# Kernel optimization log

Hardware: AMD Instinct MI355X
Metric: run time of the kernel (lower is better)

Reference implementation:

```python
import jax, jax.numpy as jnp
import numpy as np

B, S, DIM, HEADS, HD, FF = 2, 2048, 1024, 16, 64, 4096
PREV, MAX_SEQ, THETA, POS_BIAS_MAX, EPS = 1024, 4096, 10000.0, 2.0, 1e-6


def _freqs_cos_sin():
    inv = 1.0 / THETA ** (np.arange(0, HD, 2)[: HD // 2].astype(np.float32) / HD)
    f = np.outer(np.arange(MAX_SEQ, dtype=np.float32), inv)
    return jnp.asarray(np.cos(f), jnp.float32), jnp.asarray(np.sin(f), jnp.float32)


def setup_inputs():
    key = jax.random.key(0)
    ks = jax.random.split(key, 16)
    lin = lambda k, o, i: 0.02 * jax.random.normal(k, (o, i), jnp.float32)
    cos, sin = _freqs_cos_sin()
    return {
        "x": jax.random.normal(ks[0], (B, S, DIM), jnp.float32),
        "cache_k": jax.random.normal(ks[1], (B, HEADS, PREV, HD), jnp.float32),
        "cache_v": jax.random.normal(ks[2], (B, HEADS, PREV, HD), jnp.float32),
        "cos": cos, "sin": sin,
        "attn_norm_w": jnp.ones((DIM,), jnp.float32),
        "ffn_norm_w": jnp.ones((DIM,), jnp.float32),
        "wq": lin(ks[3], DIM, DIM), "bq": jnp.zeros((DIM,), jnp.float32),
        "wk": lin(ks[4], DIM, DIM), "bk": jnp.zeros((DIM,), jnp.float32),
        "wv": lin(ks[5], DIM, DIM), "bv": jnp.zeros((DIM,), jnp.float32),
        "wo": lin(ks[6], DIM, DIM), "bo": jnp.zeros((DIM,), jnp.float32),
        "w_gate": lin(ks[7], FF, DIM), "b_gate": jnp.zeros((FF,), jnp.float32),
        "w_value": lin(ks[8], FF, DIM), "b_value": jnp.zeros((FF,), jnp.float32),
        "w_proj": lin(ks[9], DIM, FF), "b_proj": jnp.zeros((DIM,), jnp.float32),
        "cache_limit": 3072,
    }


def _rmsnorm(h, w):
    return h * jax.lax.rsqrt(jnp.mean(h * h, axis=-1, keepdims=True) + EPS) * w


def _rope(t, cos, sin):
    # t: [B,H,L,HD]; cos/sin: [L, HD//2]; rotate interleaved pairs (complex mult)
    t2 = t.reshape(t.shape[:-1] + (HD // 2, 2))
    x0, x1 = t2[..., 0], t2[..., 1]
    c = cos[None, None]
    s = sin[None, None]
    out = jnp.stack([x0 * c - x1 * s, x0 * s + x1 * c], axis=-1)
    return out.reshape(t.shape)


def _forward(x, cache_k, cache_v, cos, sin, attn_norm_w, ffn_norm_w, wq, bq, wk, bk, wv, bv, wo, bo, w_gate, b_gate, w_value, b_value, w_proj, b_proj, cache_limit):
    b, s, d = x.shape
    h = _rmsnorm(x, attn_norm_w)
    shape4 = lambda t: t.reshape(b, s, HEADS, HD).transpose(0, 2, 1, 3)  # [B,H,S,HD]
    q = shape4(h @ wq.T + bq)
    k_new = shape4(h @ wk.T + bk)
    v_new = shape4(h @ wv.T + bv)
    k_all = jnp.concatenate([cache_k, k_new], axis=2)
    v_all = jnp.concatenate([cache_v, v_new], axis=2)
    if cache_limit > 0:
        k_all = k_all[:, :, -cache_limit:, :]
        v_all = v_all[:, :, -cache_limit:, :]
    total = k_all.shape[2]
    prev = total - s
    # RoPE: q at absolute positions prev..prev+s-1, keys at 0..total-1 (mod cache len)
    pos_q = (jnp.arange(s) + prev) % MAX_SEQ
    pos_k = jnp.arange(total) % MAX_SEQ
    q = _rope(q, cos[pos_q], sin[pos_q])
    k = _rope(k_all, cos[pos_k], sin[pos_k])
    # linear positional bias + causal mask over the new-token block only
    slope = POS_BIAS_MAX / max(total - 1, 1)
    j = jnp.arange(total, dtype=jnp.float32)[None, :]
    i_abs = (prev + jnp.arange(s, dtype=jnp.float32))[:, None]
    bias = slope * (j - i_abs)  # [s, total]
    causal = (jnp.arange(total)[None, :] - prev) > jnp.arange(s)[:, None]
    mask = jnp.where(causal, -jnp.inf, bias)
    scores = jnp.einsum('bhsd,bhtd->bhst', q, k) / jnp.sqrt(jnp.float32(HD)) + mask
    attn = jax.nn.softmax(scores, axis=-1)
    ctx = jnp.einsum('bhst,bhtd->bhsd', attn, v_all)
    ctx = ctx.transpose(0, 2, 1, 3).reshape(b, s, d)
    x = x + ctx @ wo.T + bo
    h2 = _rmsnorm(x, ffn_norm_w)
    gated = jax.nn.silu(h2 @ w_gate.T + b_gate) * (h2 @ w_value.T + b_value)
    return x + gated @ w_proj.T + b_proj


def reference(x, cache_k, cache_v, cos, sin, attn_norm_w, ffn_norm_w, wq, bq, wk, bk, wv, bv, wo, bo, w_gate, b_gate, w_value, b_value, w_proj, b_proj, cache_limit):
    return _forward(x, cache_k, cache_v, cos, sin, attn_norm_w, ffn_norm_w, wq, bq, wk, bk, wv, bv, wo, bo, w_gate, b_gate, w_value, b_value, w_proj, b_proj, cache_limit)
```

## Files before the change

### kernel.cpp

```cpp
#include <hip/hip_runtime.h>
#include <stdint.h>

typedef unsigned short u16;
typedef unsigned int   u32;
typedef __bf16 bf16x8 __attribute__((ext_vector_type(8)));
typedef float  f32x4  __attribute__((ext_vector_type(4)));
typedef u32    u32x4  __attribute__((ext_vector_type(4)));
typedef u32    u32x2  __attribute__((ext_vector_type(2)));

#define B_SZ  2
#define S_LEN 2048
#define NH    16
#define HD    64
#define DIM   1024
#define FF    4096
#define T_LEN 3072
#define PREV  1024
#define MROWS (B_SZ * S_LEN)
#define LOG2E 1.44269504f

#define MFMA16 __builtin_amdgcn_mfma_f32_16x16x32_bf16

__device__ __forceinline__ u16 f2bf(float f) {
  u32 u = __builtin_bit_cast(u32, f);
  u32 r = u + 0x7FFFu + ((u >> 16) & 1u);
  return (u16)(r >> 16);
}
__device__ __forceinline__ float bf2f(u16 h) {
  u32 u = ((u32)h) << 16;
  return __builtin_bit_cast(float, u);
}
__device__ __forceinline__ u32 cvtpk(float lo, float hi) {
  u32 r;
  asm("v_cvt_pk_bf16_f32 %0, %1, %2" : "=v"(r) : "v"(lo), "v"(hi));
  return r;
}

__device__ __forceinline__ void gl_lds16(const void* g, void* l) {
  __builtin_amdgcn_global_load_lds(
      (const __attribute__((address_space(1))) u32*)g,
      (__attribute__((address_space(3))) u32*)l, 16, 0, 0);
}

#define GFENCE() asm volatile("" ::: "memory")
#define BARF()                         \
  do {                                 \
    GFENCE();                          \
    __builtin_amdgcn_s_barrier();      \
    GFENCE();                          \
  } while (0)

__global__ __launch_bounds__(256) void cvt_kernel(const float* __restrict__ src,
                                                  u16* __restrict__ dst, int n4) {
  int i = blockIdx.x * 256 + threadIdx.x;
  const int stride = gridDim.x * 256;
  for (; i < n4; i += stride) {
    f32x4 v = *(const f32x4*)&src[(long)i * 4];
    u32x2 o;
    o[0] = (u32)f2bf(v[0]) | ((u32)f2bf(v[1]) << 16);
    o[1] = (u32)f2bf(v[2]) | ((u32)f2bf(v[3]) << 16);
    *(u32x2*)&dst[(long)i * 4] = o;
  }
}

__global__ __launch_bounds__(256) void cvt_sw_kernel(const float* __restrict__ src,
                                                     u16* __restrict__ dst, int nunits) {
  int i = blockIdx.x * 256 + threadIdx.x;
  const int stride = gridDim.x * 256;
  for (; i < nunits; i += stride) {
    int row = i >> 7;
    int g = i & 127;
    const float* s = &src[((long)row << 10) + g * 8];
    f32x4 a = *(const f32x4*)s;
    f32x4 b = *(const f32x4*)(s + 4);
    u32x4 o;
    o[0] = (u32)f2bf(a[0]) | ((u32)f2bf(a[1]) << 16);
    o[1] = (u32)f2bf(a[2]) | ((u32)f2bf(a[3]) << 16);
    o[2] = (u32)f2bf(b[0]) | ((u32)f2bf(b[1]) << 16);
    o[3] = (u32)f2bf(b[2]) | ((u32)f2bf(b[3]) << 16);
    const int gp = (g & ~7) | ((g & 7) ^ (row & 7));
    *(u32x4*)&dst[((long)row << 10) + gp * 8] = o;
  }
}

__global__ __launch_bounds__(256) void cvt_ilv_sw_kernel(const float* __restrict__ wg,
                                                         const float* __restrict__ wval,
                                                         u16* __restrict__ dst) {
  int i = blockIdx.x * 256 + threadIdx.x;
  const int stride = gridDim.x * 256;
  for (; i < FF * 128; i += stride) {
    int j = i >> 7;
    int g = i & 127;
    const float* sg = &wg[((long)j << 10) + g * 8];
    const float* sv = &wval[((long)j << 10) + g * 8];
    f32x4 a = *(const f32x4*)sg;
    f32x4 b = *(const f32x4*)(sg + 4);
    u32x4 og;
    og[0] = (u32)f2bf(a[0]) | ((u32)f2bf(a[1]) << 16);
    og[1] = (u32)f2bf(a[2]) | ((u32)f2bf(a[3]) << 16);
    og[2] = (u32)f2bf(b[0]) | ((u32)f2bf(b[1]) << 16);
    og[3] = (u32)f2bf(b[2]) | ((u32)f2bf(b[3]) << 16);
    f32x4 c = *(const f32x4*)sv;
    f32x4 d = *(const f32x4*)(sv + 4);
    u32x4 ov;
    ov[0] = (u32)f2bf(c[0]) | ((u32)f2bf(c[1]) << 16);
    ov[1] = (u32)f2bf(c[2]) | ((u32)f2bf(c[3]) << 16);
    ov[2] = (u32)f2bf(d[0]) | ((u32)f2bf(d[1]) << 16);
    ov[3] = (u32)f2bf(d[2]) | ((u32)f2bf(d[3]) << 16);
    const int rg = 2 * j, rv = 2 * j + 1;
    const int gpg = (g & ~7) | ((g & 7) ^ (rg & 7));
    const int gpv = (g & ~7) | ((g & 7) ^ (rv & 7));
    *(u32x4*)&dst[((long)rg << 10) + gpg * 8] = og;
    *(u32x4*)&dst[((long)rv << 10) + gpv * 8] = ov;
  }
}

__global__ __launch_bounds__(256) void bias_ilv_kernel(const float* __restrict__ bg,
                                                       const float* __restrict__ bval,
                                                       float* __restrict__ dst) {
  int i = blockIdx.x * 256 + threadIdx.x;
  if (i < FF) {
    dst[2 * i] = bg[i];
    dst[2 * i + 1] = bval[i];
  }
}

__global__ __launch_bounds__(256) void rmsnorm_kernel(const float* __restrict__ x,
                                                      const float* __restrict__ w,
                                                      u16* __restrict__ out) {
  const int row = blockIdx.x;
  const int tid = threadIdx.x;
  const long base = (long)row * DIM + tid * 4;
  f32x4 v = *(const f32x4*)&x[base];
  float ss = v[0] * v[0] + v[1] * v[1] + v[2] * v[2] + v[3] * v[3];
#pragma unroll
  for (int d = 1; d <= 32; d <<= 1) ss += __shfl_xor(ss, d, 64);
  __shared__ float red[4];
  if ((tid & 63) == 0) red[tid >> 6] = ss;
  __syncthreads();
  float tot = red[0] + red[1] + red[2] + red[3];
  const float sc = rsqrtf(tot * (1.f / (float)DIM) + 1e-6f);
  f32x4 wv4 = *(const f32x4*)&w[tid * 4];
  u32x2 o;
  o[0] = (u32)f2bf(v[0] * sc * wv4[0]) | ((u32)f2bf(v[1] * sc * wv4[1]) << 16);
  o[1] = (u32)f2bf(v[2] * sc * wv4[2]) | ((u32)f2bf(v[3] * sc * wv4[3]) << 16);
  const int u = tid >> 1, hf = tid & 1;
  const int up = (u & 0x78) | ((u & 7) ^ (row & 7));
  *(u32x2*)&out[(long)row * DIM + up * 8 + hf * 4] = o;
}

template <int EPI>
__global__ __launch_bounds__(512, 2) void gemm256(const u16* __restrict__ A,
                                                  const u16* __restrict__ Bw,
                                                  const float* __restrict__ bias,
                                                  u16* __restrict__ out_bf,
                                                  int N, int K) {
  __shared__ __align__(16) u16 Ab[2][256 * 64];
  __shared__ __align__(16) u16 Bb[2][256 * 64];
  const int tid = threadIdx.x;
  const int lane = tid & 63;
  const int wid = tid >> 6;
  const int wm = wid >> 2, wn = wid & 3;
  const int l15 = lane & 15, lhi = lane >> 4;
  const int c7 = l15 & 7;
  const long m0 = (long)blockIdx.y * 256;
  const long n0 = (long)blockIdx.x * 256;
  const int NT = K >> 6;

  const int srow = tid >> 3;
  const int sunit = (tid & 7) * 8;
  const u16* agp = A + (m0 + srow) * K + sunit;
  const u16* bgp = Bw + (n0 + srow) * K + sunit;
  const int ldst = tid * 8;

  auto stageA = [&](int kt, int b) {
    const int k0 = kt << 6;
    u16* d = &Ab[b][0];
#pragma unroll
    for (int c = 0; c < 4; ++c)
      gl_lds16(agp + (long)(c * 64) * K + k0, d + c * 4096 + ldst);
  };
  auto stageB = [&](int kt, int b) {
    const int k0 = kt << 6;
    u16* d = &Bb[b][0];
#pragma unroll
    for (int c = 0; c < 4; ++c)
      gl_lds16(bgp + (long)(c * 64) * K + k0, d + c * 4096 + ldst);
  };

#define READ_A(MH)                                                               \
  _Pragma("unroll") for (int m_ = 0; m_ < 4; ++m_) {                             \
    _Pragma("unroll") for (int ks_ = 0; ks_ < 2; ++ks_) {                        \
      Afr[MH][m_ * 2 + ks_] =                                                    \
          *(const bf16x8*)&Ac[(wm * 128 + (MH)*64 + m_ * 16 + l15) * 64 +        \
                              (((ks_ * 4 + lhi) ^ c7) * 8)];                     \
    }                                                                            \
  }
#define READ_B(NH)                                                               \
  _Pragma("unroll") for (int n_ = 0; n_ < 2; ++n_) {                             \
    _Pragma("unroll") for (int ks_ = 0; ks_ < 2; ++ks_) {                        \
      Bfr[NH][n_ * 2 + ks_] =                                                    \
          *(const bf16x8*)&Bc[(wn * 64 + (NH)*32 + n_ * 16 + l15) * 64 +         \
                              (((ks_ * 4 + lhi) ^ c7) * 8)];                     \
    }                                                                            \
  }
#define QUAD(MH, NH)                                                             \
  do {                                                                           \
    __builtin_amdgcn_s_setprio(1);                                               \
    _Pragma("unroll") for (int m_ = 0; m_ < 4; ++m_) {                           \
      _Pragma("unroll") for (int n_ = 0; n_ < 2; ++n_) {                         \
        acc[(MH)*4 + m_][(NH)*2 + n_] =                                          \
            MFMA16(Afr[MH][m_ * 2], Bfr[NH][n_ * 2],                             \
                   acc[(MH)*4 + m_][(NH)*2 + n_], 0, 0, 0);                      \
        acc[(MH)*4 + m_][(NH)*2 + n_] =                                          \
            MFMA16(Afr[MH][m_ * 2 + 1], Bfr[NH][n_ * 2 + 1],                     \
                   acc[(MH)*4 + m_][(NH)*2 + n_], 0, 0, 0);                      \
      }                                                                          \
    }                                                                            \
    __builtin_amdgcn_s_setprio(0);                                               \
  } while (0)

  f32x4 acc[8][4] = {};

  stageA(0, 0);
  stageB(0, 0);
  stageA(1, 1);
  stageB(1, 1);
  asm volatile("s_waitcnt vmcnt(8)" ::: "memory");
  __builtin_amdgcn_s_barrier();
  GFENCE();

  for (int kt = 0; kt < NT; ++kt) {
    const int b = kt & 1;
    const u16* Ac = &Ab[b][0];
    const u16* Bc = &Bb[b][0];
    bf16x8 Afr[2][8], Bfr[2][4];
    READ_A(0);
    READ_B(0);
    BARF();
    QUAD(0, 0);
    BARF();
    READ_A(1);
    READ_B(1);
    BARF();
    QUAD(0, 1);
    BARF();
    if (kt + 2 < NT) stageA(kt + 2, b);
    BARF();
    QUAD(1, 0);
    BARF();
    if (kt + 2 < NT) stageB(kt + 2, b);
    BARF();
    QUAD(1, 1);
    if (kt + 1 < NT) {
      if (kt + 2 < NT)
        asm volatile("s_waitcnt vmcnt(8)" ::: "memory");
      else
        asm volatile("s_waitcnt vmcnt(0)" ::: "memory");
      __builtin_amdgcn_s_barrier();
      GFENCE();
    }
  }
#undef READ_A
#undef READ_B
#undef QUAD

#pragma unroll
  for (int mi = 0; mi < 8; ++mi) {
    const long row0 = m0 + wm * 128 + mi * 16 + lhi * 4;
#pragma unroll
    for (int ni = 0; ni < 4; ++ni) {
      const long col = n0 + wn * 64 + ni * 16 + l15;
      const float bb = bias[col];
#pragma unroll
      for (int r = 0; r < 4; ++r) {
        float v = acc[mi][ni][r] + bb;
        if (EPI == 2) {
          float other = __shfl_xor(v, 1, 64);
          if (!(l15 & 1)) {
            float s = v / (1.f + __expf(-v)) * other;
            out_bf[(row0 + r) * (N >> 1) + (col >> 1)] = f2bf(s);
          }
        } else {
          out_bf[(row0 + r) * N + col] = f2bf(v);
        }
      }
    }
  }
}

template <int EPI, int NB>
__global__ __launch_bounds__(256) void gemm_bt(const u16* __restrict__ A,
                                               const u16* __restrict__ Bw,
                                               const float* __restrict__ bias,
                                               const float* __restrict__ resid,
                                               u16* __restrict__ out_bf,
                                               float* __restrict__ out_f,
                                               int N, int K) {
  constexpr int BHALF = NB / 64;
  constexpr int NFR = NB / 32;
  constexpr int LPT = 2 + BHALF;
  __shared__ __align__(16) u16 As[3][128 * 32];
  __shared__ __align__(16) u16 Bs[3][NB * 32];
  const int tid = threadIdx.x;
  const int lane = tid & 63;
  const int wv = tid >> 6;
  const int wr = wv >> 1, wc = wv & 1;
  const long m0 = (long)blockIdx.y * 128;
  const long n0 = (long)blockIdx.x * NB;

  const int arow = tid >> 2;
  const int acol = (tid & 3) << 3;
  const u16* ag = A + (m0 + arow) * K + acol;
  const u16* bg = Bw + (n0 + arow) * K + acol;
  const long hK = (long)64 * K;

  f32x4 acc[4][NFR] = {};
  const int l15 = lane & 15;
  const int lhi = lane >> 4;
  const int aoff0 = (wr * 64 + l15) * 32 + lhi * 8;
  const int boff0 = (wc * (NB / 2) + l15) * 32 + lhi * 8;
  const int nk = K >> 5;

  auto stage = [&](int t, int buf) {
    const int k0 = t << 5;
    gl_lds16(ag + k0, &As[buf][tid * 8]);
    gl_lds16(ag + k0 + hK, &As[buf][2048 + tid * 8]);
    gl_lds16(bg + k0, &Bs[buf][tid * 8]);
    if (BHALF == 2) gl_lds16(bg + k0 + hK, &Bs[buf][2048 + tid * 8]);
  };

  stage(0, 0);
  stage(1, 1);
  asm volatile("s_waitcnt vmcnt(%0)" ::"n"(LPT) : "memory");
  __builtin_amdgcn_s_barrier();
  GFENCE();

  for (int t = 0; t < nk; ++t) {
    const int cb = t % 3;
    if (t + 2 < nk) stage(t + 2, (t + 2) % 3);
    bf16x8 af[4], bfr[NFR];
#pragma unroll
    for (int i = 0; i < 4; ++i) af[i] = *(const bf16x8*)&As[cb][aoff0 + i * 16 * 32];
#pragma unroll
    for (int j = 0; j < NFR; ++j) bfr[j] = *(const bf16x8*)&Bs[cb][boff0 + j * 16 * 32];
    __builtin_amdgcn_s_setprio(1);
#pragma unroll
    for (int i = 0; i < 4; ++i)
#pragma unroll
      for (int j = 0; j < NFR; ++j)
        acc[i][j] = MFMA16(af[i], bfr[j], acc[i][j], 0, 0, 0);
    __builtin_amdgcn_s_setprio(0);
    if (t + 2 < nk) {
      asm volatile("s_waitcnt vmcnt(%0)" ::"n"(LPT) : "memory");
      __builtin_amdgcn_s_barrier();
      GFENCE();
    } else if (t + 1 < nk) {
      asm volatile("s_waitcnt vmcnt(0)" ::: "memory");
      __builtin_amdgcn_s_barrier();
      GFENCE();
    }
  }

#pragma unroll
  for (int i = 0; i < 4; ++i) {
    const long row0 = m0 + wr * 64 + i * 16 + lhi * 4;
#pragma unroll
    for (int j = 0; j < NFR; ++j) {
      const long col = n0 + wc * (NB / 2) + j * 16 + l15;
      const float bb = bias[col];
#pragma unroll
      for (int r = 0; r < 4; ++r) {
        const long idx = (row0 + r) * N + col;
        float v = acc[i][j][r] + bb;
        if (EPI == 0) out_bf[idx] = f2bf(v);
        else          out_f[idx] = resid[idx] + v;
      }
    }
  }
}

__global__ __launch_bounds__(256) void rope_q_kernel(const u16* __restrict__ qkv,
                                                     const float* __restrict__ cosT,
                                                     const float* __restrict__ sinT,
                                                     u16* __restrict__ Q) {
  int idx = blockIdx.x * 256 + threadIdx.x;
  int u = idx & 7;
  int s = (idx >> 3) & (S_LEN - 1);
  int bh = idx >> 14;
  int b = bh >> 4, h = bh & 15;
  int pos = PREV + s;
  const float SC = 0.125f * LOG2E;
  const u16* src = qkv + ((long)(b * S_LEN + s)) * (3 * DIM) + h * HD + u * 8;
  u32x4 d = *(const u32x4*)src;
  f32x4 cv = *(const f32x4*)&cosT[(long)pos * 32 + u * 4];
  f32x4 sv = *(const f32x4*)&sinT[(long)pos * 32 + u * 4];
  u32x4 o;
#pragma unroll
  for (int p = 0; p < 4; ++p) {
    float x0 = bf2f((u16)(d[p] & 0xffff));
    float x1 = bf2f((u16)(d[p] >> 16));
    float y0 = (x0 * cv[p] - x1 * sv[p]) * SC;
    float y1 = (x0 * sv[p] + x1 * cv[p]) * SC;
    o[p] = (u32)f2bf(y0) | ((u32)f2bf(y1) << 16);
  }
  *(u32x4*)&Q[((long)bh * S_LEN + s) * HD + u * 8] = o;
}

__global__ __launch_bounds__(256) void rope_k_kernel(const u16* __restrict__ qkv,
                                                     const float* __restrict__ cache_k,
                                                     const float* __restrict__ cosT,
                                                     const float* __restrict__ sinT,
                                                     u16* __restrict__ Kall) {
  int idx = blockIdx.x * 256 + threadIdx.x;
  int u = idx & 7;
  int t2 = idx >> 3;
  int j = t2 % T_LEN;
  int bh = t2 / T_LEN;
  int b = bh >> 4, h = bh & 15;
  float e[8];
  if (j < PREV) {
    const float* src = cache_k + ((long)bh * PREV + j) * HD + u * 8;
    f32x4 a = *(const f32x4*)src;
    f32x4 c = *(const f32x4*)(src + 4);
    e[0] = a[0]; e[1] = a[1]; e[2] = a[2]; e[3] = a[3];
    e[4] = c[0]; e[5] = c[1]; e[6] = c[2]; e[7] = c[3];
  } else {
    const u16* src = qkv + ((long)(b * S_LEN + (j - PREV))) * (3 * DIM) + DIM + h * HD + u * 8;
    u32x4 d = *(const u32x4*)src;
#pragma unroll
    for (int p = 0; p < 4; ++p) {
      e[2 * p] = bf2f((u16)(d[p] & 0xffff));
      e[2 * p + 1] = bf2f((u16)(d[p] >> 16));
    }
  }
  f32x4 cv = *(const f32x4*)&cosT[(long)j * 32 + u * 4];
  f32x4 sv = *(const f32x4*)&sinT[(long)j * 32 + u * 4];
  u32x4 o;
#pragma unroll
  for (int p = 0; p < 4; ++p) {
    float y0 = e[2 * p] * cv[p] - e[2 * p + 1] * sv[p];
    float y1 = e[2 * p] * sv[p] + e[2 * p + 1] * cv[p];
    o[p] = (u32)f2bf(y0) | ((u32)f2bf(y1) << 16);
  }
  *(u32x4*)&Kall[((long)bh * T_LEN + j) * HD + (u ^ (j & 7)) * 8] = o;
}

__global__ __launch_bounds__(256) void build_vt_kernel(const u16* __restrict__ qkv,
                                                       const float* __restrict__ cache_v,
                                                       u16* __restrict__ Vtg) {
  int idx = blockIdx.x * 256 + threadIdx.x;
  int hd = idx & 63;
  int t2 = idx >> 6;
  int kb = t2 % 384;
  int bh = t2 / 384;
  int b = bh >> 4, h = bh & 15;
  int key0 = kb * 8;
  u16 vals[8];
  if (key0 < PREV) {
#pragma unroll
    for (int i = 0; i < 8; ++i)
      vals[i] = f2bf(cache_v[((long)bh * PREV + key0 + i) * HD + hd]);
  } else {
#pragma unroll
    for (int i = 0; i < 8; ++i)
      vals[i] = qkv[((long)(b * S_LEN + key0 + i - PREV)) * (3 * DIM) + 2 * DIM + h * HD + hd];
  }
  u32x4 o;
#pragma unroll
  for (int p = 0; p < 4; ++p)
    o[p] = (u32)vals[2 * p] | ((u32)vals[2 * p + 1] << 16);
  const int span = kb >> 3;
  const int u = (kb & 7) ^ (hd & 7);
  *(u32x4*)&Vtg[((long)bh * HD + hd) * T_LEN + span * 64 + u * 8] = o;
}

__global__ __launch_bounds__(256, 2) void attn_kernel(const u16* __restrict__ Q,
                                                      const u16* __restrict__ Kg,
                                                      const u16* __restrict__ Vtg,
                                                      u16* __restrict__ ctx, float slope2) {
  __shared__ __align__(16) u16 Ks[2][64 * 64];
  __shared__ __align__(16) u16 Vs[2][64 * 64];
  __shared__ __align__(16) u16 Ps[4][16 * 64];

  const int tid = threadIdx.x;
  const int lane = tid & 63;
  const int wv = tid >> 6;
  const int l15 = lane & 15;
  const int lhi = lane >> 4;
  const int c7 = l15 & 7;
  const int bh = blockIdx.x;
  const int p = blockIdx.y;
  const int b = bh >> 4, h = bh & 15;
  const int qA0 = p * 64;
  const int qB0 = (31 - p) * 64;
  const int ntA = 17 + p;
  const int ntB = 48 - p;

  const long qrowA = (long)bh * S_LEN + qA0 + wv * 16 + l15;
  const long qrowB = (long)bh * S_LEN + qB0 + wv * 16 + l15;
  bf16x8 aqA0 = *(const bf16x8*)&Q[qrowA * HD + lhi * 8];
  bf16x8 aqA1 = *(const bf16x8*)&Q[qrowA * HD + 32 + lhi * 8];
  bf16x8 aqB0 = *(const bf16x8*)&Q[qrowB * HD + lhi * 8];
  bf16x8 aqB1 = *(const bf16x8*)&Q[qrowB * HD + 32 + lhi * 8];

  const long kgb = (long)bh * T_LEN * HD;
  const long vgb = (long)bh * HD * T_LEN;
  const int srow = tid >> 3;
  const int sunit = (tid & 7) * 8;

  const u16* kst = Kg + kgb + (long)srow * HD + sunit;
  const u16* vst = Vtg + vgb + (long)srow * T_LEN + sunit;

  gl_lds16(kst, &Ks[0][tid * 8]);
  gl_lds16(kst + 32 * HD, &Ks[0][2048 + tid * 8]);
  gl_lds16(vst, &Vs[0][tid * 8]);
  gl_lds16(vst + (long)32 * T_LEN, &Vs[0][2048 + tid * 8]);
  kst += 64 * HD;
  vst += 64;
  __syncthreads();

  f32x4 oA[4] = {}, oB[4] = {};
  f32x4 lrunA = {0.f, 0.f, 0.f, 0.f}, lrunB = {0.f, 0.f, 0.f, 0.f};
  float mrunA = -1e30f, mrunB = -1e30f;
  const int qq = wv * 16 + l15;
  u16* Pw = &Ps[wv][0];

  f32x4 be[4];
#pragma unroll
  for (int jf = 0; jf < 4; ++jf)
#pragma unroll
    for (int r = 0; r < 4; ++r)
      be[jf][r] = slope2 * (float)(jf * 16 + 4 * lhi + r);
  const float bmax = slope2 * 63.f;

  bf16x8 vones;
#pragma unroll
  for (int e = 0; e < 8; ++e) vones[e] = (__bf16)1.0f;

  float ktf = 0.f;
  const float kstep = slope2 * 64.f;

  auto process = [&](f32x4 (&sf)[4], bool maskNow, f32x4 (&o)[4], f32x4& lrun,
                     float& mrun, bf16x8 (&vf)[8]) {
    if (maskNow) {
#pragma unroll
      for (int jf = 0; jf < 4; ++jf)
#pragma unroll
        for (int r = 0; r < 4; ++r)
          if (jf * 16 + 4 * lhi + r > qq) sf[jf][r] = -1e30f;
    }
    float h0 = fmaxf(fmaxf(sf[0][0], sf[0][1]), fmaxf(sf[0][2], sf[0][3]));
    float h1 = fmaxf(fmaxf(sf[1][0], sf[1][1]), fmaxf(sf[1][2], sf[1][3]));
    float h2 = fmaxf(fmaxf(sf[2][0], sf[2][1]), fmaxf(sf[2][2], sf[2][3]));
    float h3 = fmaxf(fmaxf(sf[3][0], sf[3][1]), fmaxf(sf[3][2], sf[3][3]));
    float pm = fmaxf(fmaxf(h0, h1), fmaxf(h2, h3));
    pm = fmaxf(pm, __shfl_xor(pm, 16, 64));
    pm = fmaxf(pm, __shfl_xor(pm, 32, 64));
    const float pmax_abs = pm + ktf + bmax;

    if (!__all(pmax_abs - mrun <= 8.f)) {
      const float mnew = fmaxf(mrun, pmax_abs);
      const float scl = exp2f(mrun - mnew);
      mrun = mnew;
#pragma unroll
      for (int r = 0; r < 4; ++r) {
        const float sr = __shfl(scl, 4 * lhi + r, 64);
        lrun[r] *= sr;
#pragma unroll
        for (int hf = 0; hf < 4; ++hf) o[hf][r] *= sr;
      }
    }
    const float meff = mrun - ktf;

#pragma unroll
    for (int jf = 0; jf < 4; ++jf) {
      f32x4 pp;
#pragma unroll
      for (int r = 0; r < 4; ++r)
        pp[r] = exp2f(sf[jf][r] + (be[jf][r] - meff));
      u32x2 pw2;
      pw2[0] = cvtpk(pp[0], pp[1]);
      pw2[1] = cvtpk(pp[2], pp[3]);
      const int u = (2 * jf + (lhi >> 1)) ^ c7;
      *(u32x2*)&Pw[l15 * 64 + u * 8 + (lhi & 1) * 4] = pw2;
    }

    bf16x8 pa0 = *(const bf16x8*)&Pw[l15 * 64 + ((lhi ^ c7) * 8)];
    bf16x8 pa1 = *(const bf16x8*)&Pw[l15 * 64 + (((4 + lhi) ^ c7) * 8)];
    f32x4 psum = {};
    __builtin_amdgcn_s_setprio(1);
    psum = MFMA16(pa0, vones, psum, 0, 0, 0);
    psum = MFMA16(pa1, vones, psum, 0, 0, 0);
#pragma unroll
    for (int hf = 0; hf < 4; ++hf) {
      o[hf] = MFMA16(pa0, vf[2 * hf], o[hf], 0, 0, 0);
      o[hf] = MFMA16(pa1, vf[2 * hf + 1], o[hf], 0, 0, 0);
    }
    __builtin_amdgcn_s_setprio(0);
    lrun += psum;
  };

  for (int t = 0; t < ntB; ++t) {
    const int cur = t & 1, nxt = cur ^ 1;
    const bool lastStage = (t + 1 == ntB);
    if (!lastStage) {
      gl_lds16(kst, &Ks[nxt][tid * 8]);
      gl_lds16(kst + 32 * HD, &Ks[nxt][2048 + tid * 8]);
      gl_lds16(vst, &Vs[nxt][tid * 8]);
      gl_lds16(vst + (long)32 * T_LEN, &Vs[nxt][2048 + tid * 8]);
      kst += 64 * HD;
      vst += 64;
    }
    const bool actA = (t < ntA);

    bf16x8 kf[8];
#pragma unroll
    for (int jf = 0; jf < 4; ++jf) {
      const int krow = jf * 16 + l15;
      kf[2 * jf] = *(const bf16x8*)&Ks[cur][krow * 64 + ((lhi ^ c7) * 8)];
      kf[2 * jf + 1] = *(const bf16x8*)&Ks[cur][krow * 64 + (((4 + lhi) ^ c7) * 8)];
    }
    bf16x8 vf[8];
#pragma unroll
    for (int hf = 0; hf < 4; ++hf) {
      const int vrow = hf * 16 + l15;
      vf[2 * hf] = *(const bf16x8*)&Vs[cur][vrow * 64 + ((lhi ^ c7) * 8)];
      vf[2 * hf + 1] = *(const bf16x8*)&Vs[cur][vrow * 64 + (((4 + lhi) ^ c7) * 8)];
    }

    f32x4 sB[4], sA[4];
    __builtin_amdgcn_s_setprio(1);
#pragma unroll
    for (int jf = 0; jf < 4; ++jf) {
      f32x4 s = {};
      s = MFMA16(kf[2 * jf], aqB0, s, 0, 0, 0);
      s = MFMA16(kf[2 * jf + 1], aqB1, s, 0, 0, 0);
      sB[jf] = s;
    }
    __builtin_amdgcn_s_setprio(0);
    if (actA) {
      __builtin_amdgcn_s_setprio(1);
#pragma unroll
      for (int jf = 0; jf < 4; ++jf) {
        f32x4 s = {};
        s = MFMA16(kf[2 * jf], aqA0, s, 0, 0, 0);
        s = MFMA16(kf[2 * jf + 1], aqA1, s, 0, 0, 0);
        sA[jf] = s;
      }
      __builtin_amdgcn_s_setprio(0);
    }

    process(sB, t == ntB - 1, oB, lrunB, mrunB, vf);
    if (actA) process(sA, t == ntA - 1, oA, lrunA, mrunA, vf);

    ktf += kstep;
    if (!lastStage) __syncthreads();
  }

#pragma unroll
  for (int r = 0; r < 4; ++r) {
    const float invA = 1.f / lrunA[r];
    const float invB = 1.f / lrunB[r];
    const long rowA = (long)b * S_LEN + qA0 + wv * 16 + 4 * lhi + r;
    const long rowB = (long)b * S_LEN + qB0 + wv * 16 + 4 * lhi + r;
#pragma unroll
    for (int hf = 0; hf < 4; ++hf) {
      ctx[rowA * DIM + h * HD + hf * 16 + l15] = f2bf(oA[hf][r] * invA);
      ctx[rowB * DIM + h * HD + hf * 16 + l15] = f2bf(oB[hf][r] * invB);
    }
  }
}

extern "C" void kernel_launch(void* const* d_in, const int* in_sizes, int n_in,
                              void* d_out, int out_size, void* d_ws, size_t ws_size,
                              hipStream_t stream) {
  (void)in_sizes; (void)n_in; (void)out_size; (void)ws_size;
  const float* x       = (const float*)d_in[0];
  const float* cache_k = (const float*)d_in[1];
  const float* cache_v = (const float*)d_in[2];
  const float* cosT    = (const float*)d_in[3];
  const float* sinT    = (const float*)d_in[4];
  const float* attn_w  = (const float*)d_in[5];
  const float* ffn_w   = (const float*)d_in[6];
  const float* wq      = (const float*)d_in[7];
  const float* bq      = (const float*)d_in[8];
  const float* wk      = (const float*)d_in[9];
  const float* bk      = (const float*)d_in[10];
  const float* wv_     = (const float*)d_in[11];
  const float* bv      = (const float*)d_in[12];
  const float* wo      = (const float*)d_in[13];
  const float* bo      = (const float*)d_in[14];
  const float* wg      = (const float*)d_in[15];
  const float* bg      = (const float*)d_in[16];
  const float* wval    = (const float*)d_in[17];
  const float* bval    = (const float*)d_in[18];
  const float* wp      = (const float*)d_in[19];
  const float* bp      = (const float*)d_in[20];
  float* out = (float*)d_out;

  char* w = (char*)d_ws;
  size_t off = 0;
  auto alloc = [&](size_t bytes) -> char* {
    char* p = w + off;
    off += (bytes + 255) & ~(size_t)255;
    return p;
  };
  u16*   wqkv_bf  = (u16*)alloc((size_t)3 * DIM * DIM * 2);
  u16*   wo_bf    = (u16*)alloc((size_t)DIM * DIM * 2);
  u16*   wgv_bf   = (u16*)alloc((size_t)2 * FF * DIM * 2);
  u16*   wproj_bf = (u16*)alloc((size_t)DIM * FF * 2);
  float* bqkv     = (float*)alloc((size_t)3 * DIM * 4);
  float* bgv      = (float*)alloc((size_t)2 * FF * 4);
  float* x2       = (float*)alloc((size_t)MROWS * DIM * 4);
  char* AR = alloc((size_t)117440512);
  u16* qkv   = (u16*)(AR + 0);
  u16* Qb    = (u16*)(AR + 25165824);
  u16* Kb    = (u16*)(AR + 33554432);
  u16* Vtg   = (u16*)(AR + 46137344);
  u16* h1    = (u16*)(AR + 58720256);
  u16* ctx   = (u16*)(AR + 0);
  u16* h2    = (u16*)(AR + 8388608);
  u16* gated = (u16*)(AR + 16777216);

  cvt_sw_kernel<<<512, 256, 0, stream>>>(wq, wqkv_bf, DIM * DIM / 8);
  cvt_sw_kernel<<<512, 256, 0, stream>>>(wk, wqkv_bf + DIM * DIM, DIM * DIM / 8);
  cvt_sw_kernel<<<512, 256, 0, stream>>>(wv_, wqkv_bf + 2 * DIM * DIM, DIM * DIM / 8);
  cvt_kernel<<<512, 256, 0, stream>>>(wo, wo_bf, DIM * DIM / 4);
  cvt_ilv_sw_kernel<<<1024, 256, 0, stream>>>(wg, wval, wgv_bf);
  cvt_kernel<<<1024, 256, 0, stream>>>(wp, wproj_bf, DIM * FF / 4);
  bias_ilv_kernel<<<16, 256, 0, stream>>>(bg, bval, bgv);
  hipMemcpyAsync(bqkv, bq, DIM * 4, hipMemcpyDeviceToDevice, stream);
  hipMemcpyAsync(bqkv + DIM, bk, DIM * 4, hipMemcpyDeviceToDevice, stream);
  hipMemcpyAsync(bqkv + 2 * DIM, bv, DIM * 4, hipMemcpyDeviceToDevice, stream);

  rmsnorm_kernel<<<MROWS, 256, 0, stream>>>(x, attn_w, h1);
  gemm256<0><<<dim3(12, 16), 512, 0, stream>>>(h1, wqkv_bf, bqkv, qkv, 3 * DIM, DIM);
  rope_q_kernel<<<2048, 256, 0, stream>>>(qkv, cosT, sinT, Qb);
  rope_k_kernel<<<3072, 256, 0, stream>>>(qkv, cache_k, cosT, sinT, Kb);
  build_vt_kernel<<<3072, 256, 0, stream>>>(qkv, cache_v, Vtg);
  attn_kernel<<<dim3(B_SZ * NH, 16), 256, 0, stream>>>(
      Qb, Kb, Vtg, ctx, (2.0f / (float)(T_LEN - 1)) * LOG2E);
  gemm_bt<1, 64><<<dim3(16, 32), 256, 0, stream>>>(ctx, wo_bf, bo, x, nullptr, x2,
                                                   DIM, DIM);
  rmsnorm_kernel<<<MROWS, 256, 0, stream>>>(x2, ffn_w, h2);
  gemm256<2><<<dim3(32, 16), 512, 0, stream>>>(h2, wgv_bf, bgv, gated, 2 * FF, DIM);
  gemm_bt<1, 64><<<dim3(16, 32), 256, 0, stream>>>(gated, wproj_bf, bp, x2, nullptr, out,
                                                   DIM, FF);
}
```

Measured before the change: 372.6 us.

## Merge prep kernels, swizzle GEMM block order, double-buffer attention P tile

Folds the three QKV weight conversions into one kernel and the bias memcpys plus interleave into one pack kernel. The rope Q, rope K and V-transpose kernels become one launch that dispatches by block index. This cuts launch count and per-launch overhead. Separately, gemm256 remaps block IDs in an XCD-aware swizzle to improve L2 locality, and attention gives the A and B query streams separate P scratch buffers in LDS. That doubles the Ps footprint and may affect occupancy.

```diff
diff --git a/kernel.cpp b/kernel.cpp
--- a/kernel.cpp
+++ b/kernel.cpp
@@ -63,13 +63,18 @@
   }
 }
 
-__global__ __launch_bounds__(256) void cvt_sw_kernel(const float* __restrict__ src,
-                                                     u16* __restrict__ dst, int nunits) {
+__global__ __launch_bounds__(256) void cvt_qkv_sw_kernel(const float* __restrict__ wq,
+                                                         const float* __restrict__ wk,
+                                                         const float* __restrict__ wv,
+                                                         u16* __restrict__ dst) {
   int i = blockIdx.x * 256 + threadIdx.x;
   const int stride = gridDim.x * 256;
-  for (; i < nunits; i += stride) {
-    int row = i >> 7;
-    int g = i & 127;
+  for (; i < 3 * 131072; i += stride) {
+    const int seg = i >> 17;
+    const int loc = i & 131071;
+    const float* src = (seg == 0) ? wq : (seg == 1) ? wk : wv;
+    int row = loc >> 7;
+    int g = loc & 127;
     const float* s = &src[((long)row << 10) + g * 8];
     f32x4 a = *(const f32x4*)s;
     f32x4 b = *(const f32x4*)(s + 4);
@@ -79,7 +84,7 @@
     o[2] = (u32)f2bf(b[0]) | ((u32)f2bf(b[1]) << 16);
     o[3] = (u32)f2bf(b[2]) | ((u32)f2bf(b[3]) << 16);
     const int gp = (g & ~7) | ((g & 7) ^ (row & 7));
-    *(u32x4*)&dst[((long)row << 10) + gp * 8] = o;
+    *(u32x4*)&dst[((long)seg << 20) + ((long)row << 10) + gp * 8] = o;
   }
 }
 
@@ -115,13 +120,21 @@
   }
 }
 
-__global__ __launch_bounds__(256) void bias_ilv_kernel(const float* __restrict__ bg,
-                                                       const float* __restrict__ bval,
-                                                       float* __restrict__ dst) {
+__global__ __launch_bounds__(256) void bias_pack_kernel(const float* __restrict__ bq,
+                                                        const float* __restrict__ bk,
+                                                        const float* __restrict__ bv,
+                                                        const float* __restrict__ bg,
+                                                        const float* __restrict__ bval,
+                                                        float* __restrict__ bqkv,
+                                                        float* __restrict__ bgv) {
   int i = blockIdx.x * 256 + threadIdx.x;
-  if (i < FF) {
-    dst[2 * i] = bg[i];
-    dst[2 * i + 1] = bval[i];
+  if (i < 3 * DIM) {
+    float v = (i < DIM) ? bq[i] : (i < 2 * DIM) ? bk[i - DIM] : bv[i - 2 * DIM];
+    bqkv[i] = v;
+  } else if (i < 3 * DIM + FF) {
+    int j = i - 3 * DIM;
+    bgv[2 * j] = bg[j];
+    bgv[2 * j + 1] = bval[j];
   }
 }
 
@@ -163,8 +176,12 @@
   const int wm = wid >> 2, wn = wid & 3;
   const int l15 = lane & 15, lhi = lane >> 4;
   const int c7 = l15 & 7;
-  const long m0 = (long)blockIdx.y * 256;
-  const long n0 = (long)blockIdx.x * 256;
+  const int nwg = gridDim.x * gridDim.y;
+  const int id = blockIdx.y * gridDim.x + blockIdx.x;
+  const int cpx = nwg >> 3;
+  const int swz = (id & 7) * cpx + (id >> 3);
+  const long m0 = (long)(swz / gridDim.x) * 256;
+  const long n0 = (long)(swz % gridDim.x) * 256;
   const int NT = K >> 6;
 
   const int srow = tid >> 3;
@@ -380,99 +397,96 @@
   }
 }
 
-__global__ __launch_bounds__(256) void rope_q_kernel(const u16* __restrict__ qkv,
-                                                     const float* __restrict__ cosT,
-                                                     const float* __restrict__ sinT,
-                                                     u16* __restrict__ Q) {
-  int idx = blockIdx.x * 256 + threadIdx.x;
-  int u = idx & 7;
-  int s = (idx >> 3) & (S_LEN - 1);
-  int bh = idx >> 14;
-  int b = bh >> 4, h = bh & 15;
-  int pos = PREV + s;
-  const float SC = 0.125f * LOG2E;
-  const u16* src = qkv + ((long)(b * S_LEN + s)) * (3 * DIM) + h * HD + u * 8;
-  u32x4 d = *(const u32x4*)src;
-  f32x4 cv = *(const f32x4*)&cosT[(long)pos * 32 + u * 4];
-  f32x4 sv = *(const f32x4*)&sinT[(long)pos * 32 + u * 4];
-  u32x4 o;
-#pragma unroll
-  for (int p = 0; p < 4; ++p) {
-    float x0 = bf2f((u16)(d[p] & 0xffff));
-    float x1 = bf2f((u16)(d[p] >> 16));
-    float y0 = (x0 * cv[p] - x1 * sv[p]) * SC;
-    float y1 = (x0 * sv[p] + x1 * cv[p]) * SC;
-    o[p] = (u32)f2bf(y0) | ((u32)f2bf(y1) << 16);
-  }
-  *(u32x4*)&Q[((long)bh * S_LEN + s) * HD + u * 8] = o;
-}
-
-__global__ __launch_bounds__(256) void rope_k_kernel(const u16* __restrict__ qkv,
-                                                     const float* __restrict__ cache_k,
-                                                     const float* __restrict__ cosT,
-                                                     const float* __restrict__ sinT,
-                                                     u16* __restrict__ Kall) {
-  int idx = blockIdx.x * 256 + threadIdx.x;
-  int u = idx & 7;
-  int t2 = idx >> 3;
-  int j = t2 % T_LEN;
-  int bh = t2 / T_LEN;
-  int b = bh >> 4, h = bh & 15;
-  float e[8];
-  if (j < PREV) {
-    const float* src = cache_k + ((long)bh * PREV + j) * HD + u * 8;
-    f32x4 a = *(const f32x4*)src;
-    f32x4 c = *(const f32x4*)(src + 4);
-    e[0] = a[0]; e[1] = a[1]; e[2] = a[2]; e[3] = a[3];
-    e[4] = c[0]; e[5] = c[1]; e[6] = c[2]; e[7] = c[3];
+__global__ __launch_bounds__(256) void rope_all_kernel(const u16* __restrict__ qkv,
+                                                       const float* __restrict__ cache_k,
+                                                       const float* __restrict__ cache_v,
+                                                       const float* __restrict__ cosT,
+                                                       const float* __restrict__ sinT,
+                                                       u16* __restrict__ Q,
+                                                       u16* __restrict__ Kall,
+                                                       u16* __restrict__ Vtg) {
+  const int blk = blockIdx.x;
+  if (blk < 2048) {
+    int idx = blk * 256 + threadIdx.x;
+    int u = idx & 7;
+    int s = (idx >> 3) & (S_LEN - 1);
+    int bh = idx >> 14;
+    int b = bh >> 4, h = bh & 15;
+    int pos = PREV + s;
+    const float SC = 0.125f * LOG2E;
+    const u16* src = qkv + ((long)(b * S_LEN + s)) * (3 * DIM) + h * HD + u * 8;
+    u32x4 d = *(const u32x4*)src;
+    f32x4 cv = *(const f32x4*)&cosT[(long)pos * 32 + u * 4];
+    f32x4 sv = *(const f32x4*)&sinT[(long)pos * 32 + u * 4];
+    u32x4 o;
+#pragma unroll
+    for (int p = 0; p < 4; ++p) {
+      float x0 = bf2f((u16)(d[p] & 0xffff));
+      float x1 = bf2f((u16)(d[p] >> 16));
+      float y0 = (x0 * cv[p] - x1 * sv[p]) * SC;
+      float y1 = (x0 * sv[p] + x1 * cv[p]) * SC;
+      o[p] = (u32)f2bf(y0) | ((u32)f2bf(y1) << 16);
+    }
+    *(u32x4*)&Q[((long)bh * S_LEN + s) * HD + u * 8] = o;
+  } else if (blk < 5120) {
+    int idx = (blk - 2048) * 256 + threadIdx.x;
+    int u = idx & 7;
+    int t2 = idx >> 3;
+    int j = t2 % T_LEN;
+    int bh = t2 / T_LEN;
+    int b = bh >> 4, h = bh & 15;
+    float e[8];
+    if (j < PREV) {
+      const float* src = cache_k + ((long)bh * PREV + j) * HD + u * 8;
+      f32x4 a = *(const f32x4*)src;
+      f32x4 c = *(const f32x4*)(src + 4);
+      e[0] = a[0]; e[1] = a[1]; e[2] = a[2]; e[3] = a[3];
+      e[4] = c[0]; e[5] = c[1]; e[6] = c[2]; e[7] = c[3];
+    } else {
+      const u16* src = qkv + ((long)(b * S_LEN + (j - PREV))) * (3 * DIM) + DIM + h * HD + u * 8;
+      u32x4 d = *(const u32x4*)src;
+#pragma unroll
+      for (int p = 0; p < 4; ++p) {
+        e[2 * p] = bf2f((u16)(d[p] & 0xffff));
+        e[2 * p + 1] = bf2f((u16)(d[p] >> 16));
+      }
+    }
+    f32x4 cv = *(const f32x4*)&cosT[(long)j * 32 + u * 4];
+    f32x4 sv = *(const f32x4*)&sinT[(long)j * 32 + u * 4];
+    u32x4 o;
+#pragma unroll
+    for (int p = 0; p < 4; ++p) {
+      float y0 = e[2 * p] * cv[p] - e[2 * p + 1] * sv[p];
+      float y1 = e[2 * p] * sv[p] + e[2 * p + 1] * cv[p];
+      o[p] = (u32)f2bf(y0) | ((u32)f2bf(y1) << 16);
+    }
+    *(u32x4*)&Kall[((long)bh * T_LEN + j) * HD + (u ^ (j & 7)) * 8] = o;
   } else {
-    const u16* src = qkv + ((long)(b * S_LEN + (j - PREV))) * (3 * DIM) + DIM + h * HD + u * 8;
-    u32x4 d = *(const u32x4*)src;
-#pragma unroll
-    for (int p = 0; p < 4; ++p) {
-      e[2 * p] = bf2f((u16)(d[p] & 0xffff));
-      e[2 * p + 1] = bf2f((u16)(d[p] >> 16));
-    }
-  }
-  f32x4 cv = *(const f32x4*)&cosT[(long)j * 32 + u * 4];
-  f32x4 sv = *(const f32x4*)&sinT[(long)j * 32 + u * 4];
-  u32x4 o;
-#pragma unroll
-  for (int p = 0; p < 4; ++p) {
-    float y0 = e[2 * p] * cv[p] - e[2 * p + 1] * sv[p];
-    float y1 = e[2 * p] * sv[p] + e[2 * p + 1] * cv[p];
-    o[p] = (u32)f2bf(y0) | ((u32)f2bf(y1) << 16);
-  }
-  *(u32x4*)&Kall[((long)bh * T_LEN + j) * HD + (u ^ (j & 7)) * 8] = o;
-}
-
-__global__ __launch_bounds__(256) void build_vt_kernel(const u16* __restrict__ qkv,
-                                                       const float* __restrict__ cache_v,
-                                                       u16* __restrict__ Vtg) {
-  int idx = blockIdx.x * 256 + threadIdx.x;
-  int hd = idx & 63;
-  int t2 = idx >> 6;
-  int kb = t2 % 384;
-  int bh = t2 / 384;
-  int b = bh >> 4, h = bh & 15;
-  int key0 = kb * 8;
-  u16 vals[8];
-  if (key0 < PREV) {
-#pragma unroll
-    for (int i = 0; i < 8; ++i)
-      vals[i] = f2bf(cache_v[((long)bh * PREV + key0 + i) * HD + hd]);
-  } else {
-#pragma unroll
-    for (int i = 0; i < 8; ++i)
-      vals[i] = qkv[((long)(b * S_LEN + key0 + i - PREV)) * (3 * DIM) + 2 * DIM + h * HD + hd];
-  }
-  u32x4 o;
-#pragma unroll
-  for (int p = 0; p < 4; ++p)
-    o[p] = (u32)vals[2 * p] | ((u32)vals[2 * p + 1] << 16);
-  const int span = kb >> 3;
-  const int u = (kb & 7) ^ (hd & 7);
-  *(u32x4*)&Vtg[((long)bh * HD + hd) * T_LEN + span * 64 + u * 8] = o;
+    int idx = (blk - 5120) * 256 + threadIdx.x;
+    int hd = idx & 63;
+    int t2 = idx >> 6;
+    int kb = t2 % 384;
+    int bh = t2 / 384;
+    int b = bh >> 4, h = bh & 15;
+    int key0 = kb * 8;
+    u16 vals[8];
+    if (key0 < PREV) {
+#pragma unroll
+      for (int i = 0; i < 8; ++i)
+        vals[i] = f2bf(cache_v[((long)bh * PREV + key0 + i) * HD + hd]);
+    } else {
+#pragma unroll
+      for (int i = 0; i < 8; ++i)
+        vals[i] = qkv[((long)(b * S_LEN + key0 + i - PREV)) * (3 * DIM) + 2 * DIM + h * HD + hd];
+    }
+    u32x4 o;
+#pragma unroll
+    for (int p = 0; p < 4; ++p)
+      o[p] = (u32)vals[2 * p] | ((u32)vals[2 * p + 1] << 16);
+    const int span = kb >> 3;
+    const int u = (kb & 7) ^ (hd & 7);
+    *(u32x4*)&Vtg[((long)bh * HD + hd) * T_LEN + span * 64 + u * 8] = o;
+  }
 }
 
 __global__ __launch_bounds__(256, 2) void attn_kernel(const u16* __restrict__ Q,
@@ -481,7 +495,7 @@
                                                       u16* __restrict__ ctx, float slope2) {
   __shared__ __align__(16) u16 Ks[2][64 * 64];
   __shared__ __align__(16) u16 Vs[2][64 * 64];
-  __shared__ __align__(16) u16 Ps[4][16 * 64];
+  __shared__ __align__(16) u16 Ps[2][4][16 * 64];
 
   const int tid = threadIdx.x;
   const int lane = tid & 63;
@@ -524,7 +538,6 @@
   f32x4 lrunA = {0.f, 0.f, 0.f, 0.f}, lrunB = {0.f, 0.f, 0.f, 0.f};
   float mrunA = -1e30f, mrunB = -1e30f;
   const int qq = wv * 16 + l15;
-  u16* Pw = &Ps[wv][0];
 
   f32x4 be[4];
 #pragma unroll
@@ -542,7 +555,7 @@
   const float kstep = slope2 * 64.f;
 
   auto process = [&](f32x4 (&sf)[4], bool maskNow, f32x4 (&o)[4], f32x4& lrun,
-                     float& mrun, bf16x8 (&vf)[8]) {
+                     float& mrun, bf16x8 (&vf)[8], u16* Pw) {
     if (maskNow) {
 #pragma unroll
       for (int jf = 0; jf < 4; ++jf)
@@ -651,8 +664,8 @@
       __builtin_amdgcn_s_setprio(0);
     }
 
-    process(sB, t == ntB - 1, oB, lrunB, mrunB, vf);
-    if (actA) process(sA, t == ntA - 1, oA, lrunA, mrunA, vf);
+    process(sB, t == ntB - 1, oB, lrunB, mrunB, vf, &Ps[0][wv][0]);
+    if (actA) process(sA, t == ntA - 1, oA, lrunA, mrunA, vf, &Ps[1][wv][0]);
 
     ktf += kstep;
     if (!lastStage) __syncthreads();
@@ -723,22 +736,16 @@
   u16* h2    = (u16*)(AR + 8388608);
   u16* gated = (u16*)(AR + 16777216);
 
-  cvt_sw_kernel<<<512, 256, 0, stream>>>(wq, wqkv_bf, DIM * DIM / 8);
-  cvt_sw_kernel<<<512, 256, 0, stream>>>(wk, wqkv_bf + DIM * DIM, DIM * DIM / 8);
-  cvt_sw_kernel<<<512, 256, 0, stream>>>(wv_, wqkv_bf + 2 * DIM * DIM, DIM * DIM / 8);
+  cvt_qkv_sw_kernel<<<1024, 256, 0, stream>>>(wq, wk, wv_, wqkv_bf);
   cvt_kernel<<<512, 256, 0, stream>>>(wo, wo_bf, DIM * DIM / 4);
   cvt_ilv_sw_kernel<<<1024, 256, 0, stream>>>(wg, wval, wgv_bf);
   cvt_kernel<<<1024, 256, 0, stream>>>(wp, wproj_bf, DIM * FF / 4);
-  bias_ilv_kernel<<<16, 256, 0, stream>>>(bg, bval, bgv);
-  hipMemcpyAsync(bqkv, bq, DIM * 4, hipMemcpyDeviceToDevice, stream);
-  hipMemcpyAsync(bqkv + DIM, bk, DIM * 4, hipMemcpyDeviceToDevice, stream);
-  hipMemcpyAsync(bqkv + 2 * DIM, bv, DIM * 4, hipMemcpyDeviceToDevice, stream);
+  bias_pack_kernel<<<28, 256, 0, stream>>>(bq, bk, bv, bg, bval, bqkv, bgv);
 
   rmsnorm_kernel<<<MROWS, 256, 0, stream>>>(x, attn_w, h1);
   gemm256<0><<<dim3(12, 16), 512, 0, stream>>>(h1, wqkv_bf, bqkv, qkv, 3 * DIM, DIM);
-  rope_q_kernel<<<2048, 256, 0, stream>>>(qkv, cosT, sinT, Qb);
-  rope_k_kernel<<<3072, 256, 0, stream>>>(qkv, cache_k, cosT, sinT, Kb);
-  build_vt_kernel<<<3072, 256, 0, stream>>>(qkv, cache_v, Vtg);
+  rope_all_kernel<<<8192, 256, 0, stream>>>(qkv, cache_k, cache_v, cosT, sinT,
+                                            Qb, Kb, Vtg);
   attn_kernel<<<dim3(B_SZ * NH, 16), 256, 0, stream>>>(
       Qb, Kb, Vtg, ctx, (2.0f / (float)(T_LEN - 1)) * LOG2E);
   gemm_bt<1, 64><<<dim3(16, 32), 256, 0, stream>>>(ctx, wo_bf, bo, x, nullptr, x2,
```

After: 361.1 us. -3.1%, faster.
